# Kernel optimization log

Measured on AMD Instinct MI355X. Metric: run time of the kernel, lower is better.

The kernel has to match this reference:

```python
import jax, jax.numpy as jnp
import numpy as np

N_EMBD = 768
N_HEAD = 12
HEAD_SIZE = N_EMBD // N_HEAD
LN_EPS = 1e-5


def setup_inputs() -> dict:
    key = jax.random.key(0)
    ks = jax.random.split(key, 12)
    s = 0.02
    B, T, C = 8, 1024, N_EMBD
    return {
        "x":  jax.random.normal(ks[0], (B, T, C), dtype=jnp.float32),
        # per-head q/k/v projections packed as [C, H*hs] (concat of head outputs)
        "Wq": jax.random.normal(ks[1], (C, C), dtype=jnp.float32) * s,
        "Wk": jax.random.normal(ks[2], (C, C), dtype=jnp.float32) * s,
        "Wv": jax.random.normal(ks[3], (C, C), dtype=jnp.float32) * s,
        "Wo": jax.random.normal(ks[4], (C, C), dtype=jnp.float32) * s,
        "bo": jnp.zeros((C,), dtype=jnp.float32),
        "W1": jax.random.normal(ks[5], (C, 4 * C), dtype=jnp.float32) * s,
        "b1": jnp.zeros((4 * C,), dtype=jnp.float32),
        "W2": jax.random.normal(ks[6], (4 * C, C), dtype=jnp.float32) * s,
        "b2": jnp.zeros((C,), dtype=jnp.float32),
        "g1": jnp.ones((C,), dtype=jnp.float32),
        "be1": jnp.zeros((C,), dtype=jnp.float32),
        "g2": jnp.ones((C,), dtype=jnp.float32),
        "be2": jnp.zeros((C,), dtype=jnp.float32),
    }


def _layernorm(x, g, b):
    mu = jnp.mean(x, axis=-1, keepdims=True)
    var = jnp.mean(jnp.square(x - mu), axis=-1, keepdims=True)
    return (x - mu) * jax.lax.rsqrt(var + LN_EPS) * g + b


def _block(x, Wq, Wk, Wv, Wo, bo, W1, b1, W2, b2, g1, be1, g2, be2):
    B, T, C = x.shape
    H, hs = N_HEAD, HEAD_SIZE
    h = _layernorm(x, g1, be1)
    q = (h @ Wq).reshape(B, T, H, hs)
    k = (h @ Wk).reshape(B, T, H, hs)
    v = (h @ Wv).reshape(B, T, H, hs)
    # NOTE: original code scales by n_embd**-0.5 (C from x.shape), not head_size**-0.5
    scores = jnp.einsum("bthd,bshd->bhts", q, k) * (C ** -0.5)
    causal = jnp.tril(jnp.ones((T, T), dtype=bool))  # [T,T]
    scores = jnp.where(causal, scores, -jnp.inf)
    attn = jax.nn.softmax(scores, axis=-1)  # [B,H,T,T]
    o = jnp.einsum("bhts,bshd->bthd", attn, v).reshape(B, T, C)
    x = x + o @ Wo + bo
    h2 = _layernorm(x, g2, be2)
    ff = jax.nn.gelu(h2 @ W1 + b1, approximate=False) @ W2 + b2
    return x + ff


def reference(x, Wq, Wk, Wv, Wo, bo, W1, b1, W2, b2, g1, be1, g2, be2):
    return _block(x, Wq, Wk, Wv, Wo, bo, W1, b1, W2, b2, g1, be1, g2, be2)
```

## Files before the change

kernel.cpp:

```cpp
#include <hip/hip_runtime.h>
#include <math.h>
#include <stdint.h>

typedef unsigned short u16;
typedef unsigned int u32;
typedef __attribute__((ext_vector_type(8))) __bf16 bf16x8;
typedef __attribute__((ext_vector_type(4))) float f32x4;

#define AS1 __attribute__((address_space(1)))
#define AS3 __attribute__((address_space(3)))

__device__ __forceinline__ void stage16(const void* g, void* l) {
    __builtin_amdgcn_global_load_lds((const AS1 void*)(uintptr_t)g,
                                     (AS3 void*)(uintptr_t)l, 16, 0, 0);
}

__device__ __forceinline__ u16 f2bf(float f) {
    u32 u = __float_as_uint(f);
    u += 0x7fffu + ((u >> 16) & 1u);
    return (u16)(u >> 16);
}

__device__ __forceinline__ float bf2f(u16 v) {
    u32 u = ((u32)v) << 16;
    return __uint_as_float(u);
}

__global__ __launch_bounds__(256) void ln_kernel(const float* __restrict__ x,
                                                 const float* __restrict__ g,
                                                 const float* __restrict__ b,
                                                 u16* __restrict__ out) {
    __shared__ float s8[8];
    int row = blockIdx.x;
    int tid = threadIdx.x;
    const int w = tid >> 6;
    const float* xr = x + (size_t)row * 768;
    float x0 = xr[tid], x1 = xr[tid + 256], x2 = xr[tid + 512];

    float sum = x0 + x1 + x2;
#pragma unroll
    for (int off = 32; off; off >>= 1) sum += __shfl_xor(sum, off);
    if ((tid & 63) == 0) s8[w] = sum;
    __syncthreads();
    float mu = (s8[0] + s8[1] + s8[2] + s8[3]) * (1.0f / 768.0f);

    float d0 = x0 - mu, d1 = x1 - mu, d2 = x2 - mu;
    float sq = d0 * d0 + d1 * d1 + d2 * d2;
#pragma unroll
    for (int off = 32; off; off >>= 1) sq += __shfl_xor(sq, off);
    if ((tid & 63) == 0) s8[4 + w] = sq;
    __syncthreads();
    float var = (s8[4] + s8[5] + s8[6] + s8[7]) * (1.0f / 768.0f);
    float rs = rsqrtf(var + 1e-5f);

    u16* orow = out + (size_t)row * 768;
    orow[tid]       = f2bf(d0 * rs * g[tid]       + b[tid]);
    orow[tid + 256] = f2bf(d1 * rs * g[tid + 256] + b[tid + 256]);
    orow[tid + 512] = f2bf(d2 * rs * g[tid + 512] + b[tid + 512]);
}

__global__ __launch_bounds__(256) void transpose_bf16(const float* __restrict__ W,
                                                      u16* __restrict__ Wt,
                                                      int K, int N) {
    __shared__ float t[32][33];
    int tx = threadIdx.x, ty = threadIdx.y;
    int n0 = blockIdx.x * 32, k0 = blockIdx.y * 32;
#pragma unroll
    for (int j = 0; j < 32; j += 8)
        t[ty + j][tx] = W[(size_t)(k0 + ty + j) * N + n0 + tx];
    __syncthreads();
#pragma unroll
    for (int j = 0; j < 32; j += 8)
        Wt[(size_t)(n0 + ty + j) * K + k0 + tx] = f2bf(t[tx][ty + j]);
}

__global__ __launch_bounds__(256) void transpose4_768(const float* __restrict__ Wq,
                                                      const float* __restrict__ Wk,
                                                      const float* __restrict__ Wv,
                                                      const float* __restrict__ Wo,
                                                      u16* __restrict__ Wqkvt,
                                                      u16* __restrict__ Wot) {
    __shared__ float t[32][33];
    const int z = blockIdx.z;
    const float* W = (z == 0) ? Wq : (z == 1) ? Wk : (z == 2) ? Wv : Wo;
    u16* Wt = (z == 3) ? Wot : (Wqkvt + (size_t)z * 768 * 768);
    int tx = threadIdx.x, ty = threadIdx.y;
    int n0 = blockIdx.x * 32, k0 = blockIdx.y * 32;
#pragma unroll
    for (int j = 0; j < 32; j += 8)
        t[ty + j][tx] = W[(size_t)(k0 + ty + j) * 768 + n0 + tx];
    __syncthreads();
#pragma unroll
    for (int j = 0; j < 32; j += 8)
        Wt[(size_t)(n0 + ty + j) * 768 + k0 + tx] = f2bf(t[tx][ty + j]);
}

__global__ __launch_bounds__(256) void vt_kernel(const u16* __restrict__ qkv,
                                                 u16* __restrict__ Vt) {
    __shared__ u16 t[32][34];
    const int tx = threadIdx.x, ty = threadIdx.y;
    const int s0 = blockIdx.x * 32, d0 = blockIdx.y * 32, bh = blockIdx.z;
    const int b = bh / 12, h = bh % 12;
#pragma unroll
    for (int j = 0; j < 32; j += 8)
        t[ty + j][tx] = qkv[((size_t)(b * 1024) + s0 + ty + j) * 2304 + 1536 + h * 64 + d0 + tx];
    __syncthreads();
#pragma unroll
    for (int j = 0; j < 32; j += 8)
        Vt[((size_t)bh * 64 + d0 + ty + j) * 1024 + s0 + tx] = t[tx][ty + j];
}

__global__ __launch_bounds__(256, 3) void gemm_k32(
    const u16* __restrict__ A, const u16* __restrict__ Bt,
    const float* __restrict__ bias, const float* __restrict__ res,
    float* __restrict__ outF, u16* __restrict__ outB,
    int N, int K, int act) {
    __shared__ char lds[49152];
    const int tid = threadIdx.x, lane = tid & 63, wid = tid >> 6;
    const int l15 = lane & 15, lk = lane >> 4;
    const int wrow = (wid >> 1) * 64, wcol = (wid & 1) * 64;

    int wg = blockIdx.y * gridDim.x + blockIdx.x;
    const int nwg = gridDim.x * gridDim.y;
    wg = (wg & 7) * (nwg >> 3) + (wg >> 3);
    const int brow = (wg / gridDim.x) * 128;
    const int bcol = (wg % gridDim.x) * 128;

    const size_t K2 = (size_t)K * 2;
    const char* Abase = (const char*)A + (size_t)brow * K2;
    const char* Bbase = (const char*)Bt + (size_t)bcol * K2;

    int srow[2], scol[2];
#pragma unroll
    for (int j = 0; j < 2; ++j) {
        const int L = j * 4096 + tid * 16;
        srow[j] = L >> 6;
        scol[j] = (L & 63) ^ (((srow[j] >> 1) & 3) << 4);
    }

    const int nt = K >> 5;

    auto stage_tile = [&](int t, char* dst) {
#pragma unroll
        for (int j = 0; j < 2; ++j) {
            const size_t off = (size_t)srow[j] * K2 + (size_t)t * 64 + scol[j];
            stage16(Abase + off, dst + j * 4096 + tid * 16);
            stage16(Bbase + off, dst + 8192 + j * 4096 + tid * 16);
        }
    };

    f32x4 acc[4][4] = {};

    stage_tile(0, lds);
    stage_tile(1, lds + 16384);

    auto iter = [&](int t, char* buf, char* nxt) {
        if (t + 1 < nt) asm volatile("s_waitcnt vmcnt(4)\n\ts_barrier" ::: "memory");
        else            asm volatile("s_waitcnt vmcnt(0)\n\ts_barrier" ::: "memory");
        __builtin_amdgcn_sched_barrier(0);

        if (t + 2 < nt) stage_tile(t + 2, nxt);

        const char* As = buf;
        const char* Bs = buf + 8192;
        bf16x8 af[4], bfv[4];
#pragma unroll
        for (int m = 0; m < 4; ++m) {
            const int row = wrow + m * 16 + l15;
            af[m] = *(const bf16x8*)(As + row * 64 +
                                     ((lk * 16) ^ (((row >> 1) & 3) << 4)));
        }
#pragma unroll
        for (int n = 0; n < 4; ++n) {
            const int row = wcol + n * 16 + l15;
            bfv[n] = *(const bf16x8*)(Bs + row * 64 +
                                      ((lk * 16) ^ (((row >> 1) & 3) << 4)));
        }
        __builtin_amdgcn_s_setprio(1);
#pragma unroll
        for (int m = 0; m < 4; ++m)
#pragma unroll
            for (int n = 0; n < 4; ++n)
                acc[m][n] = __builtin_amdgcn_mfma_f32_16x16x32_bf16(af[m], bfv[n], acc[m][n], 0, 0, 0);
        __builtin_amdgcn_s_setprio(0);
    };

    for (int t = 0; t < nt; t += 3) {
        iter(t,     lds,         lds + 32768);
        iter(t + 1, lds + 16384, lds);
        iter(t + 2, lds + 32768, lds + 16384);
    }

#pragma unroll
    for (int m = 0; m < 4; ++m)
#pragma unroll
        for (int n = 0; n < 4; ++n)
#pragma unroll
            for (int r = 0; r < 4; ++r) {
                int row = brow + wrow + m * 16 + lk * 4 + r;
                int col = bcol + wcol + n * 16 + l15;
                float v = acc[m][n][r];
                if (bias) v += bias[col];
                if (act) v = 0.5f * v * (1.0f + erff(v * 0.70710678118654752f));
                if (res) v += res[(size_t)row * N + col];
                if (outB) outB[(size_t)row * N + col] = f2bf(v);
                else outF[(size_t)row * N + col] = v;
            }
}

__global__ __launch_bounds__(256, 3) void gemm_splitk(
    const u16* __restrict__ A, const u16* __restrict__ Bt,
    u16* __restrict__ p0, u16* __restrict__ p1, int N, int K) {
    __shared__ char lds[49152];
    const int tid = threadIdx.x, lane = tid & 63, wid = tid >> 6;
    const int l15 = lane & 15, lk = lane >> 4;
    const int wrow = (wid >> 1) * 64, wcol = (wid & 1) * 64;
    const int z = blockIdx.z;
    const int Kh = K >> 1;

    int wg = blockIdx.y * gridDim.x + blockIdx.x;
    const int nwg = gridDim.x * gridDim.y;
    wg = (wg & 7) * (nwg >> 3) + (wg >> 3);
    const int brow = (wg / gridDim.x) * 128;
    const int bcol = (wg % gridDim.x) * 128;

    const size_t K2 = (size_t)K * 2;
    const char* Abase = (const char*)A + (size_t)brow * K2 + (size_t)z * Kh * 2;
    const char* Bbase = (const char*)Bt + (size_t)bcol * K2 + (size_t)z * Kh * 2;

    int srow[2], scol[2];
#pragma unroll
    for (int j = 0; j < 2; ++j) {
        const int L = j * 4096 + tid * 16;
        srow[j] = L >> 6;
        scol[j] = (L & 63) ^ (((srow[j] >> 1) & 3) << 4);
    }

    const int nt = Kh >> 5;

    auto stage_tile = [&](int t, char* dst) {
#pragma unroll
        for (int j = 0; j < 2; ++j) {
            const size_t off = (size_t)srow[j] * K2 + (size_t)t * 64 + scol[j];
            stage16(Abase + off, dst + j * 4096 + tid * 16);
            stage16(Bbase + off, dst + 8192 + j * 4096 + tid * 16);
        }
    };

    f32x4 acc[4][4] = {};

    stage_tile(0, lds);
    stage_tile(1, lds + 16384);

    auto iter = [&](int t, char* buf, char* nxt) {
        if (t + 1 < nt) asm volatile("s_waitcnt vmcnt(4)\n\ts_barrier" ::: "memory");
        else            asm volatile("s_waitcnt vmcnt(0)\n\ts_barrier" ::: "memory");
        __builtin_amdgcn_sched_barrier(0);

        if (t + 2 < nt) stage_tile(t + 2, nxt);

        const char* As = buf;
        const char* Bs = buf + 8192;
        bf16x8 af[4], bfv[4];
#pragma unroll
        for (int m = 0; m < 4; ++m) {
            const int row = wrow + m * 16 + l15;
            af[m] = *(const bf16x8*)(As + row * 64 +
                                     ((lk * 16) ^ (((row >> 1) & 3) << 4)));
        }
#pragma unroll
        for (int n = 0; n < 4; ++n) {
            const int row = wcol + n * 16 + l15;
            bfv[n] = *(const bf16x8*)(Bs + row * 64 +
                                      ((lk * 16) ^ (((row >> 1) & 3) << 4)));
        }
        __builtin_amdgcn_s_setprio(1);
#pragma unroll
        for (int m = 0; m < 4; ++m)
#pragma unroll
            for (int n = 0; n < 4; ++n)
                acc[m][n] = __builtin_amdgcn_mfma_f32_16x16x32_bf16(af[m], bfv[n], acc[m][n], 0, 0, 0);
        __builtin_amdgcn_s_setprio(0);
    };

    for (int t = 0; t < nt; t += 3) {
        iter(t,     lds,         lds + 32768);
        iter(t + 1, lds + 16384, lds);
        iter(t + 2, lds + 32768, lds + 16384);
    }

    u16* outP = z ? p1 : p0;
#pragma unroll
    for (int m = 0; m < 4; ++m)
#pragma unroll
        for (int n = 0; n < 4; ++n)
#pragma unroll
            for (int r = 0; r < 4; ++r) {
                int row = brow + wrow + m * 16 + lk * 4 + r;
                int col = bcol + wcol + n * 16 + l15;
                outP[(size_t)row * N + col] = f2bf(acc[m][n][r]);
            }
}

__global__ __launch_bounds__(256) void ff2_reduce(const float* __restrict__ x2,
                                                  const float* __restrict__ b2,
                                                  const u16* __restrict__ p0,
                                                  const u16* __restrict__ p1,
                                                  float* __restrict__ out) {
    const size_t i = ((size_t)blockIdx.x * 256 + threadIdx.x) * 4;
    const float4 a = *(const float4*)(x2 + i);
    const int col = (int)(i % 768);
    const float4 bb = *(const float4*)(b2 + col);
    const ushort4 q0 = *(const ushort4*)(p0 + i);
    const ushort4 q1 = *(const ushort4*)(p1 + i);
    float4 o;
    o.x = a.x + bb.x + bf2f(q0.x) + bf2f(q1.x);
    o.y = a.y + bb.y + bf2f(q0.y) + bf2f(q1.y);
    o.z = a.z + bb.z + bf2f(q0.z) + bf2f(q1.z);
    o.w = a.w + bb.w + bf2f(q0.w) + bf2f(q1.w);
    *(float4*)(out + i) = o;
}

__global__ __launch_bounds__(256) void attn_mfma(const u16* __restrict__ qkv,
                                                 const u16* __restrict__ Vt,
                                                 u16* __restrict__ obf) {
    __shared__ char lds[40960];
    const int tid = threadIdx.x, lane = tid & 63, w = tid >> 6;
    const int g = lane >> 4, l15 = lane & 15;

    int wg = blockIdx.y * gridDim.x + blockIdx.x;
    const int nwg = gridDim.x * gridDim.y;
    wg = (wg & 7) * (nwg >> 3) + (wg >> 3);
    const int qb = 15 - (wg & 15);
    const int bh = wg >> 4;
    const int h = bh % 12, b = bh / 12;
    const int t0 = qb * 64;
    const float scale = 0.03608439182435161f;

    const size_t qrow = ((size_t)b * 1024 + t0 + 16 * w + l15) * 2304 + h * 64;
    const bf16x8 qf0 = *(const bf16x8*)(qkv + qrow + 8 * g);
    const bf16x8 qf1 = *(const bf16x8*)(qkv + qrow + 8 * g + 32);

    const int sub = ((lane & 7) * 16) ^ ((lane >> 3) << 4);
    const int r0 = 16 * w + (lane >> 3);
    const char* kSrc = (const char*)qkv + ((size_t)(b * 1024 + r0) * 2304 + 768 + h * 64) * 2 + sub;
    const char* vSrc = (const char*)Vt + ((size_t)(bh * 64 + r0) * 1024) * 2 + sub;
    const int dstOff = 2 * w * 1024 + lane * 16;

    stage16(kSrc,            lds + dstOff);
    stage16(kSrc + 8 * 4608, lds + dstOff + 1024);
    stage16(vSrc,            lds + 8192 + dstOff);
    stage16(vSrc + 8 * 2048, lds + 8192 + dstOff + 1024);
    kSrc += 64 * 4608; vSrc += 128;
    __syncthreads();

    const int swzA = (l15 & 7) << 4;
    float m_r[4] = {-1e30f, -1e30f, -1e30f, -1e30f};
    float l_r[4] = {0.f, 0.f, 0.f, 0.f};
    f32x4 oacc[4] = {};
    char* Pw = lds + 32768 + w * 2048;

    for (int c = 0; c <= qb; ++c) {
        if (c < qb) {
            char* dst = lds + ((c + 1) & 1) * 16384;
            stage16(kSrc,            dst + dstOff);
            stage16(kSrc + 8 * 4608, dst + dstOff + 1024);
            stage16(vSrc,            dst + 8192 + dstOff);
            stage16(vSrc + 8 * 2048, dst + 8192 + dstOff + 1024);
            kSrc += 64 * 4608; vSrc += 128;
            asm volatile("s_waitcnt vmcnt(4)\n\ts_barrier" ::: "memory");
        } else {
            asm volatile("s_waitcnt vmcnt(0)\n\ts_barrier" ::: "memory");
        }
        __builtin_amdgcn_sched_barrier(0);

        const char* bufK = lds + (c & 1) * 16384;
        const char* bufV = bufK + 8192;

        f32x4 sacc[4] = {};
#pragma unroll
        for (int st = 0; st < 4; ++st) {
            const char* krow = bufK + (l15 + 16 * st) * 128;
            const bf16x8 kf0 = *(const bf16x8*)(krow + ((16 * g) ^ swzA));
            const bf16x8 kf1 = *(const bf16x8*)(krow + ((16 * g + 64) ^ swzA));
            sacc[st] = __builtin_amdgcn_mfma_f32_16x16x32_bf16(qf0, kf0, sacc[st], 0, 0, 0);
            sacc[st] = __builtin_amdgcn_mfma_f32_16x16x32_bf16(qf1, kf1, sacc[st], 0, 0, 0);
        }

        const bool diag = (c == qb);
#pragma unroll
        for (int r = 0; r < 4; ++r) {
            float sv0 = sacc[0][r] * scale, sv1 = sacc[1][r] * scale;
            float sv2 = sacc[2][r] * scale, sv3 = sacc[3][r] * scale;
            if (diag) {
                const int trel = 16 * w + 4 * g + r;
                if (l15 +  0 > trel) sv0 = -1e30f;
                if (l15 + 16 > trel) sv1 = -1e30f;
                if (l15 + 32 > trel) sv2 = -1e30f;
                if (l15 + 48 > trel) sv3 = -1e30f;
            }
            float mx = fmaxf(fmaxf(sv0, sv1), fmaxf(sv2, sv3));
#pragma unroll
            for (int off = 1; off < 16; off <<= 1) mx = fmaxf(mx, __shfl_xor(mx, off));
            if (mx > m_r[r]) {
                const float corr = __expf(m_r[r] - mx);
                m_r[r] = mx;
                l_r[r] *= corr;
                oacc[0][r] *= corr; oacc[1][r] *= corr;
                oacc[2][r] *= corr; oacc[3][r] *= corr;
            }
            const float p0 = __expf(sv0 - m_r[r]), p1 = __expf(sv1 - m_r[r]);
            const float p2 = __expf(sv2 - m_r[r]), p3 = __expf(sv3 - m_r[r]);
            float ps = p0 + p1 + p2 + p3;
#pragma unroll
            for (int off = 1; off < 16; off <<= 1) ps += __shfl_xor(ps, off);
            l_r[r] += ps;
            const int q = 4 * g + r;
            char* pr = Pw + q * 128;
            const int sw = (q & 7) << 4;
            *(u16*)(pr + ((l15 * 2 +  0) ^ sw)) = f2bf(p0);
            *(u16*)(pr + ((l15 * 2 + 32) ^ sw)) = f2bf(p1);
            *(u16*)(pr + ((l15 * 2 + 64) ^ sw)) = f2bf(p2);
            *(u16*)(pr + ((l15 * 2 + 96) ^ sw)) = f2bf(p3);
        }

#pragma unroll
        for (int kc = 0; kc < 2; ++kc) {
            const bf16x8 pa = *(const bf16x8*)(Pw + l15 * 128 + ((16 * g + 64 * kc) ^ swzA));
#pragma unroll
            for (int dt = 0; dt < 4; ++dt) {
                const int d = l15 + 16 * dt;
                const bf16x8 vf = *(const bf16x8*)(bufV + d * 128 +
                                   ((16 * g + 64 * kc) ^ ((d & 7) << 4)));
                oacc[dt] = __builtin_amdgcn_mfma_f32_16x16x32_bf16(pa, vf, oacc[dt], 0, 0, 0);
            }
        }
        asm volatile("s_barrier" ::: "memory");
    }

    const size_t orow0 = ((size_t)b * 1024 + t0 + 16 * w) * 768 + h * 64;
#pragma unroll
    for (int r = 0; r < 4; ++r) {
        const float inv = 1.0f / l_r[r];
        const size_t orow = orow0 + (size_t)(4 * g + r) * 768;
#pragma unroll
        for (int dt = 0; dt < 4; ++dt)
            obf[orow + 16 * dt + l15] = f2bf(oacc[dt][r] * inv);
    }
}

extern "C" void kernel_launch(void* const* d_in, const int* in_sizes, int n_in,
                              void* d_out, int out_size, void* d_ws, size_t ws_size,
                              hipStream_t stream) {
    const float* x   = (const float*)d_in[0];
    const float* Wq  = (const float*)d_in[1];
    const float* Wk  = (const float*)d_in[2];
    const float* Wv  = (const float*)d_in[3];
    const float* Wo  = (const float*)d_in[4];
    const float* bo  = (const float*)d_in[5];
    const float* W1  = (const float*)d_in[6];
    const float* b1  = (const float*)d_in[7];
    const float* W2  = (const float*)d_in[8];
    const float* b2  = (const float*)d_in[9];
    const float* g1  = (const float*)d_in[10];
    const float* be1 = (const float*)d_in[11];
    const float* g2  = (const float*)d_in[12];
    const float* be2 = (const float*)d_in[13];
    float* out = (float*)d_out;

    char* ws = (char*)d_ws;
    u16* qkv_bf = (u16*)(ws);
    u16* ff1_bf = (u16*)(ws);
    float* x2   = (float*)(ws + 50331648);
    u16* h_bf   = (u16*)(ws + 75497472);
    u16* o_bf   = (u16*)(ws + 88080384);
    u16* p0_bf  = h_bf;
    u16* p1_bf  = o_bf;
    u16* Wqkvt  = (u16*)(ws + 100663296);
    u16* W1t    = (u16*)(ws + 104202240);
    u16* W2t    = (u16*)(ws + 108920832);
    u16* Wot    = (u16*)(ws + 113639424);
    u16* Vt     = (u16*)(ws + 114819072);

    dim3 tb(32, 8);
    transpose4_768<<<dim3(24, 24, 4), tb, 0, stream>>>(Wq, Wk, Wv, Wo, Wqkvt, Wot);
    transpose_bf16<<<dim3(96, 24), tb, 0, stream>>>(W1, W1t, 768, 3072);
    transpose_bf16<<<dim3(24, 96), tb, 0, stream>>>(W2, W2t, 3072, 768);

    ln_kernel<<<8192, 256, 0, stream>>>(x, g1, be1, h_bf);
    gemm_k32<<<dim3(18, 64), 256, 0, stream>>>(h_bf, Wqkvt, nullptr, nullptr, nullptr, qkv_bf, 2304, 768, 0);
    vt_kernel<<<dim3(32, 2, 96), tb, 0, stream>>>(qkv_bf, Vt);
    attn_mfma<<<dim3(16, 96), 256, 0, stream>>>(qkv_bf, Vt, o_bf);
    gemm_k32<<<dim3(6, 64), 256, 0, stream>>>(o_bf, Wot, bo, x, x2, nullptr, 768, 768, 0);
    ln_kernel<<<8192, 256, 0, stream>>>(x2, g2, be2, h_bf);
    gemm_k32<<<dim3(24, 64), 256, 0, stream>>>(h_bf, W1t, b1, nullptr, nullptr, ff1_bf, 3072, 768, 1);
    gemm_splitk<<<dim3(6, 64, 2), 256, 0, stream>>>(ff1_bf, W2t, p0_bf, p1_bf, 768, 3072);
    ff2_reduce<<<6144, 256, 0, stream>>>(x2, b2, p0_bf, p1_bf, out);
}
```

Baseline: 347.0 us.

## Pair causal query blocks per attention workgroup and widen FFN1 GEMM tile

The attention kernel now gives each workgroup two query blocks (p and 15-p) processed one after the other, so every workgroup does an equal amount of causal work and the grid is halved. A new gemm_x2 kernel computes a 128x256 output tile per workgroup for the W1 projection, reusing each A fragment across two B tiles and cutting the number of workgroups. The trade-offs are fewer workgroups with more serial work each, plus higher register pressure in gemm_x2 (two accumulator sets, launch bounds lowered to 2 waves per SIMD).

Result: faster. 330.3 us (-4.8%).

```diff
diff --git a/kernel.cpp b/kernel.cpp
--- a/kernel.cpp
+++ b/kernel.cpp
@@ -205,6 +205,117 @@
                 if (res) v += res[(size_t)row * N + col];
                 if (outB) outB[(size_t)row * N + col] = f2bf(v);
                 else outF[(size_t)row * N + col] = v;
+            }
+}
+
+__global__ __launch_bounds__(256, 2) void gemm_x2(
+    const u16* __restrict__ A, const u16* __restrict__ Bt,
+    const float* __restrict__ bias, u16* __restrict__ outB,
+    int N, int K, int act) {
+    __shared__ char lds[49152];
+    const int tid = threadIdx.x, lane = tid & 63, wid = tid >> 6;
+    const int l15 = lane & 15, lk = lane >> 4;
+    const int wrow = (wid >> 1) * 64, wcol = (wid & 1) * 64;
+
+    int wg = blockIdx.y * gridDim.x + blockIdx.x;
+    const int nwg = gridDim.x * gridDim.y;
+    wg = (wg & 7) * (nwg >> 3) + (wg >> 3);
+    const int brow = (wg / gridDim.x) * 128;
+    const int bcol = (wg % gridDim.x) * 256;
+
+    const size_t K2 = (size_t)K * 2;
+    const char* Abase  = (const char*)A + (size_t)brow * K2;
+    const char* B0base = (const char*)Bt + (size_t)bcol * K2;
+    const char* B1base = (const char*)Bt + (size_t)(bcol + 128) * K2;
+
+    int srow[2], scol[2];
+#pragma unroll
+    for (int j = 0; j < 2; ++j) {
+        const int L = j * 4096 + tid * 16;
+        srow[j] = L >> 6;
+        scol[j] = (L & 63) ^ (((srow[j] >> 1) & 3) << 4);
+    }
+
+    const int nt = K >> 5;
+
+    auto stage_tile = [&](int t, char* dst) {
+#pragma unroll
+        for (int j = 0; j < 2; ++j) {
+            const size_t off = (size_t)srow[j] * K2 + (size_t)t * 64 + scol[j];
+            stage16(Abase + off,  dst + j * 4096 + tid * 16);
+            stage16(B0base + off, dst + 8192 + j * 4096 + tid * 16);
+            stage16(B1base + off, dst + 16384 + j * 4096 + tid * 16);
+        }
+    };
+
+    f32x4 acc0[4][4] = {};
+    f32x4 acc1[4][4] = {};
+
+    stage_tile(0, lds);
+
+    for (int t = 0; t < nt; ++t) {
+        if (t + 1 < nt) {
+            stage_tile(t + 1, lds + ((t + 1) & 1) * 24576);
+            asm volatile("s_waitcnt vmcnt(6)\n\ts_barrier" ::: "memory");
+        } else {
+            asm volatile("s_waitcnt vmcnt(0)\n\ts_barrier" ::: "memory");
+        }
+        __builtin_amdgcn_sched_barrier(0);
+
+        const char* buf = lds + (t & 1) * 24576;
+        bf16x8 af[4], bfv[4];
+#pragma unroll
+        for (int m = 0; m < 4; ++m) {
+            const int row = wrow + m * 16 + l15;
+            af[m] = *(const bf16x8*)(buf + row * 64 +
+                                     ((lk * 16) ^ (((row >> 1) & 3) << 4)));
+        }
+#pragma unroll
+        for (int n = 0; n < 4; ++n) {
+            const int row = wcol + n * 16 + l15;
+            bfv[n] = *(const bf16x8*)(buf + 8192 + row * 64 +
+                                      ((lk * 16) ^ (((row >> 1) & 3) << 4)));
+        }
+        __builtin_amdgcn_s_setprio(1);
+#pragma unroll
+        for (int m = 0; m < 4; ++m)
+#pragma unroll
+            for (int n = 0; n < 4; ++n)
+                acc0[m][n] = __builtin_amdgcn_mfma_f32_16x16x32_bf16(af[m], bfv[n], acc0[m][n], 0, 0, 0);
+        __builtin_amdgcn_s_setprio(0);
+#pragma unroll
+        for (int n = 0; n < 4; ++n) {
+            const int row = wcol + n * 16 + l15;
+            bfv[n] = *(const bf16x8*)(buf + 16384 + row * 64 +
+                                      ((lk * 16) ^ (((row >> 1) & 3) << 4)));
+        }
+        __builtin_amdgcn_s_setprio(1);
+#pragma unroll
+        for (int m = 0; m < 4; ++m)
+#pragma unroll
+            for (int n = 0; n < 4; ++n)
+                acc1[m][n] = __builtin_amdgcn_mfma_f32_16x16x32_bf16(af[m], bfv[n], acc1[m][n], 0, 0, 0);
+        __builtin_amdgcn_s_setprio(0);
+        __builtin_amdgcn_s_barrier();
+    }
+
+#pragma unroll
+    for (int m = 0; m < 4; ++m)
+#pragma unroll
+        for (int n = 0; n < 4; ++n)
+#pragma unroll
+            for (int r = 0; r < 4; ++r) {
+                int row = brow + wrow + m * 16 + lk * 4 + r;
+                int col = bcol + wcol + n * 16 + l15;
+                float v0 = acc0[m][n][r];
+                float v1 = acc1[m][n][r];
+                if (bias) { v0 += bias[col]; v1 += bias[col + 128]; }
+                if (act) {
+                    v0 = 0.5f * v0 * (1.0f + erff(v0 * 0.70710678118654752f));
+                    v1 = 0.5f * v1 * (1.0f + erff(v1 * 0.70710678118654752f));
+                }
+                outB[(size_t)row * N + col]       = f2bf(v0);
+                outB[(size_t)row * N + col + 128] = f2bf(v1);
             }
 }
 
@@ -331,121 +442,127 @@
     int wg = blockIdx.y * gridDim.x + blockIdx.x;
     const int nwg = gridDim.x * gridDim.y;
     wg = (wg & 7) * (nwg >> 3) + (wg >> 3);
-    const int qb = 15 - (wg & 15);
-    const int bh = wg >> 4;
+    const int p = wg / 96;
+    const int bh = wg % 96;
     const int h = bh % 12, b = bh / 12;
-    const int t0 = qb * 64;
     const float scale = 0.03608439182435161f;
-
-    const size_t qrow = ((size_t)b * 1024 + t0 + 16 * w + l15) * 2304 + h * 64;
-    const bf16x8 qf0 = *(const bf16x8*)(qkv + qrow + 8 * g);
-    const bf16x8 qf1 = *(const bf16x8*)(qkv + qrow + 8 * g + 32);
 
     const int sub = ((lane & 7) * 16) ^ ((lane >> 3) << 4);
     const int r0 = 16 * w + (lane >> 3);
-    const char* kSrc = (const char*)qkv + ((size_t)(b * 1024 + r0) * 2304 + 768 + h * 64) * 2 + sub;
-    const char* vSrc = (const char*)Vt + ((size_t)(bh * 64 + r0) * 1024) * 2 + sub;
     const int dstOff = 2 * w * 1024 + lane * 16;
-
-    stage16(kSrc,            lds + dstOff);
-    stage16(kSrc + 8 * 4608, lds + dstOff + 1024);
-    stage16(vSrc,            lds + 8192 + dstOff);
-    stage16(vSrc + 8 * 2048, lds + 8192 + dstOff + 1024);
-    kSrc += 64 * 4608; vSrc += 128;
-    __syncthreads();
-
     const int swzA = (l15 & 7) << 4;
-    float m_r[4] = {-1e30f, -1e30f, -1e30f, -1e30f};
-    float l_r[4] = {0.f, 0.f, 0.f, 0.f};
-    f32x4 oacc[4] = {};
     char* Pw = lds + 32768 + w * 2048;
 
-    for (int c = 0; c <= qb; ++c) {
-        if (c < qb) {
-            char* dst = lds + ((c + 1) & 1) * 16384;
-            stage16(kSrc,            dst + dstOff);
-            stage16(kSrc + 8 * 4608, dst + dstOff + 1024);
-            stage16(vSrc,            dst + 8192 + dstOff);
-            stage16(vSrc + 8 * 2048, dst + 8192 + dstOff + 1024);
-            kSrc += 64 * 4608; vSrc += 128;
-            asm volatile("s_waitcnt vmcnt(4)\n\ts_barrier" ::: "memory");
-        } else {
-            asm volatile("s_waitcnt vmcnt(0)\n\ts_barrier" ::: "memory");
-        }
-        __builtin_amdgcn_sched_barrier(0);
-
-        const char* bufK = lds + (c & 1) * 16384;
-        const char* bufV = bufK + 8192;
-
-        f32x4 sacc[4] = {};
-#pragma unroll
-        for (int st = 0; st < 4; ++st) {
-            const char* krow = bufK + (l15 + 16 * st) * 128;
-            const bf16x8 kf0 = *(const bf16x8*)(krow + ((16 * g) ^ swzA));
-            const bf16x8 kf1 = *(const bf16x8*)(krow + ((16 * g + 64) ^ swzA));
-            sacc[st] = __builtin_amdgcn_mfma_f32_16x16x32_bf16(qf0, kf0, sacc[st], 0, 0, 0);
-            sacc[st] = __builtin_amdgcn_mfma_f32_16x16x32_bf16(qf1, kf1, sacc[st], 0, 0, 0);
-        }
-
-        const bool diag = (c == qb);
+#pragma unroll 1
+    for (int half = 0; half < 2; ++half) {
+        const int qb = half ? p : (15 - p);
+        const int t0 = qb * 64;
+
+        const size_t qrow = ((size_t)b * 1024 + t0 + 16 * w + l15) * 2304 + h * 64;
+        const bf16x8 qf0 = *(const bf16x8*)(qkv + qrow + 8 * g);
+        const bf16x8 qf1 = *(const bf16x8*)(qkv + qrow + 8 * g + 32);
+
+        const char* kSrc = (const char*)qkv + ((size_t)(b * 1024 + r0) * 2304 + 768 + h * 64) * 2 + sub;
+        const char* vSrc = (const char*)Vt + ((size_t)(bh * 64 + r0) * 1024) * 2 + sub;
+
+        stage16(kSrc,            lds + dstOff);
+        stage16(kSrc + 8 * 4608, lds + dstOff + 1024);
+        stage16(vSrc,            lds + 8192 + dstOff);
+        stage16(vSrc + 8 * 2048, lds + 8192 + dstOff + 1024);
+        kSrc += 64 * 4608; vSrc += 128;
+        __syncthreads();
+
+        float m_r[4] = {-1e30f, -1e30f, -1e30f, -1e30f};
+        float l_r[4] = {0.f, 0.f, 0.f, 0.f};
+        f32x4 oacc[4] = {};
+
+        for (int c = 0; c <= qb; ++c) {
+            if (c < qb) {
+                char* dst = lds + ((c + 1) & 1) * 16384;
+                stage16(kSrc,            dst + dstOff);
+                stage16(kSrc + 8 * 4608, dst + dstOff + 1024);
+                stage16(vSrc,            dst + 8192 + dstOff);
+                stage16(vSrc + 8 * 2048, dst + 8192 + dstOff + 1024);
+                kSrc += 64 * 4608; vSrc += 128;
+                asm volatile("s_waitcnt vmcnt(4)\n\ts_barrier" ::: "memory");
+            } else {
+                asm volatile("s_waitcnt vmcnt(0)\n\ts_barrier" ::: "memory");
+            }
+            __builtin_amdgcn_sched_barrier(0);
+
+            const char* bufK = lds + (c & 1) * 16384;
+            const char* bufV = bufK + 8192;
+
+            f32x4 sacc[4] = {};
+#pragma unroll
+            for (int st = 0; st < 4; ++st) {
+                const char* krow = bufK + (l15 + 16 * st) * 128;
+                const bf16x8 kf0 = *(const bf16x8*)(krow + ((16 * g) ^ swzA));
+                const bf16x8 kf1 = *(const bf16x8*)(krow + ((16 * g + 64) ^ swzA));
+                sacc[st] = __builtin_amdgcn_mfma_f32_16x16x32_bf16(qf0, kf0, sacc[st], 0, 0, 0);
+                sacc[st] = __builtin_amdgcn_mfma_f32_16x16x32_bf16(qf1, kf1, sacc[st], 0, 0, 0);
+            }
+
+            const bool diag = (c == qb);
+#pragma unroll
+            for (int r = 0; r < 4; ++r) {
+                float sv0 = sacc[0][r] * scale, sv1 = sacc[1][r] * scale;
+                float sv2 = sacc[2][r] * scale, sv3 = sacc[3][r] * scale;
+                if (diag) {
+                    const int trel = 16 * w + 4 * g + r;
+                    if (l15 +  0 > trel) sv0 = -1e30f;
+                    if (l15 + 16 > trel) sv1 = -1e30f;
+                    if (l15 + 32 > trel) sv2 = -1e30f;
+                    if (l15 + 48 > trel) sv3 = -1e30f;
+                }
+                float mx = fmaxf(fmaxf(sv0, sv1), fmaxf(sv2, sv3));
+#pragma unroll
+                for (int off = 1; off < 16; off <<= 1) mx = fmaxf(mx, __shfl_xor(mx, off));
+                if (mx > m_r[r]) {
+                    const float corr = __expf(m_r[r] - mx);
+                    m_r[r] = mx;
+                    l_r[r] *= corr;
+                    oacc[0][r] *= corr; oacc[1][r] *= corr;
+                    oacc[2][r] *= corr; oacc[3][r] *= corr;
+                }
+                const float p0 = __expf(sv0 - m_r[r]), p1 = __expf(sv1 - m_r[r]);
+                const float p2 = __expf(sv2 - m_r[r]), p3 = __expf(sv3 - m_r[r]);
+                float ps = p0 + p1 + p2 + p3;
+#pragma unroll
+                for (int off = 1; off < 16; off <<= 1) ps += __shfl_xor(ps, off);
+                l_r[r] += ps;
+                const int q = 4 * g + r;
+                char* pr = Pw + q * 128;
+                const int sw = (q & 7) << 4;
+                *(u16*)(pr + ((l15 * 2 +  0) ^ sw)) = f2bf(p0);
+                *(u16*)(pr + ((l15 * 2 + 32) ^ sw)) = f2bf(p1);
+                *(u16*)(pr + ((l15 * 2 + 64) ^ sw)) = f2bf(p2);
+                *(u16*)(pr + ((l15 * 2 + 96) ^ sw)) = f2bf(p3);
+            }
+
+#pragma unroll
+            for (int kc = 0; kc < 2; ++kc) {
+                const bf16x8 pa = *(const bf16x8*)(Pw + l15 * 128 + ((16 * g + 64 * kc) ^ swzA));
+#pragma unroll
+                for (int dt = 0; dt < 4; ++dt) {
+                    const int d = l15 + 16 * dt;
+                    const bf16x8 vf = *(const bf16x8*)(bufV + d * 128 +
+                                       ((16 * g + 64 * kc) ^ ((d & 7) << 4)));
+                    oacc[dt] = __builtin_amdgcn_mfma_f32_16x16x32_bf16(pa, vf, oacc[dt], 0, 0, 0);
+                }
+            }
+            asm volatile("s_barrier" ::: "memory");
+        }
+
+        const size_t orow0 = ((size_t)b * 1024 + t0 + 16 * w) * 768 + h * 64;
 #pragma unroll
         for (int r = 0; r < 4; ++r) {
-            float sv0 = sacc[0][r] * scale, sv1 = sacc[1][r] * scale;
-            float sv2 = sacc[2][r] * scale, sv3 = sacc[3][r] * scale;
-            if (diag) {
-                const int trel = 16 * w + 4 * g + r;
-                if (l15 +  0 > trel) sv0 = -1e30f;
-                if (l15 + 16 > trel) sv1 = -1e30f;
-                if (l15 + 32 > trel) sv2 = -1e30f;
-                if (l15 + 48 > trel) sv3 = -1e30f;
-            }
-            float mx = fmaxf(fmaxf(sv0, sv1), fmaxf(sv2, sv3));
-#pragma unroll
-            for (int off = 1; off < 16; off <<= 1) mx = fmaxf(mx, __shfl_xor(mx, off));
-            if (mx > m_r[r]) {
-                const float corr = __expf(m_r[r] - mx);
-                m_r[r] = mx;
-                l_r[r] *= corr;
-                oacc[0][r] *= corr; oacc[1][r] *= corr;
-                oacc[2][r] *= corr; oacc[3][r] *= corr;
-            }
-            const float p0 = __expf(sv0 - m_r[r]), p1 = __expf(sv1 - m_r[r]);
-            const float p2 = __expf(sv2 - m_r[r]), p3 = __expf(sv3 - m_r[r]);
-            float ps = p0 + p1 + p2 + p3;
-#pragma unroll
-            for (int off = 1; off < 16; off <<= 1) ps += __shfl_xor(ps, off);
-            l_r[r] += ps;
-            const int q = 4 * g + r;
-            char* pr = Pw + q * 128;
-            const int sw = (q & 7) << 4;
-            *(u16*)(pr + ((l15 * 2 +  0) ^ sw)) = f2bf(p0);
-            *(u16*)(pr + ((l15 * 2 + 32) ^ sw)) = f2bf(p1);
-            *(u16*)(pr + ((l15 * 2 + 64) ^ sw)) = f2bf(p2);
-            *(u16*)(pr + ((l15 * 2 + 96) ^ sw)) = f2bf(p3);
-        }
-
-#pragma unroll
-        for (int kc = 0; kc < 2; ++kc) {
-            const bf16x8 pa = *(const bf16x8*)(Pw + l15 * 128 + ((16 * g + 64 * kc) ^ swzA));
-#pragma unroll
-            for (int dt = 0; dt < 4; ++dt) {
-                const int d = l15 + 16 * dt;
-                const bf16x8 vf = *(const bf16x8*)(bufV + d * 128 +
-                                   ((16 * g + 64 * kc) ^ ((d & 7) << 4)));
-                oacc[dt] = __builtin_amdgcn_mfma_f32_16x16x32_bf16(pa, vf, oacc[dt], 0, 0, 0);
-            }
-        }
-        asm volatile("s_barrier" ::: "memory");
-    }
-
-    const size_t orow0 = ((size_t)b * 1024 + t0 + 16 * w) * 768 + h * 64;
-#pragma unroll
-    for (int r = 0; r < 4; ++r) {
-        const float inv = 1.0f / l_r[r];
-        const size_t orow = orow0 + (size_t)(4 * g + r) * 768;
-#pragma unroll
-        for (int dt = 0; dt < 4; ++dt)
-            obf[orow + 16 * dt + l15] = f2bf(oacc[dt][r] * inv);
+            const float inv = 1.0f / l_r[r];
+            const size_t orow = orow0 + (size_t)(4 * g + r) * 768;
+#pragma unroll
+            for (int dt = 0; dt < 4; ++dt)
+                obf[orow + 16 * dt + l15] = f2bf(oacc[dt][r] * inv);
+        }
     }
 }
 
@@ -490,10 +607,10 @@
     ln_kernel<<<8192, 256, 0, stream>>>(x, g1, be1, h_bf);
     gemm_k32<<<dim3(18, 64), 256, 0, stream>>>(h_bf, Wqkvt, nullptr, nullptr, nullptr, qkv_bf, 2304, 768, 0);
     vt_kernel<<<dim3(32, 2, 96), tb, 0, stream>>>(qkv_bf, Vt);
-    attn_mfma<<<dim3(16, 96), 256, 0, stream>>>(qkv_bf, Vt, o_bf);
+    attn_mfma<<<dim3(8, 96), 256, 0, stream>>>(qkv_bf, Vt, o_bf);
     gemm_k32<<<dim3(6, 64), 256, 0, stream>>>(o_bf, Wot, bo, x, x2, nullptr, 768, 768, 0);
     ln_kernel<<<8192, 256, 0, stream>>>(x2, g2, be2, h_bf);
-    gemm_k32<<<dim3(24, 64), 256, 0, stream>>>(h_bf, W1t, b1, nullptr, nullptr, ff1_bf, 3072, 768, 1);
+    gemm_x2<<<dim3(12, 64), 256, 0, stream>>>(h_bf, W1t, b1, ff1_bf, 3072, 768, 1);
     gemm_splitk<<<dim3(6, 64, 2), 256, 0, stream>>>(ff1_bf, W2t, p0_bf, p1_bf, 768, 3072);
     ff2_reduce<<<6144, 256, 0, stream>>>(x2, b2, p0_bf, p1_bf, out);
 }
```

## Pair causal query blocks per workgroup and stage GEMM bf16 epilogues through LDS

Applied to the files above, without the earlier changes.

The attention kernel now gives each workgroup two query blocks, p and 15-p, processed one after the other. This balances the causal triangle's work across workgroups and halves the grid. The bf16-output GEMM epilogues (gemm_k32 with outB, and split-K) now write the tile into LDS first, then store it to global memory as coalesced 16-byte rows instead of scattered 2-byte stores. The cost is an extra LDS round trip and a barrier, a longer serial loop per attention workgroup, and fewer attention workgroups to fill the GPU.

New measurement: 308.2 us. -11.2%, faster.

```diff
diff --git a/kernel.cpp b/kernel.cpp
--- a/kernel.cpp
+++ b/kernel.cpp
@@ -191,21 +191,45 @@
         iter(t + 2, lds + 32768, lds + 16384);
     }
 
-#pragma unroll
-    for (int m = 0; m < 4; ++m)
-#pragma unroll
-        for (int n = 0; n < 4; ++n)
-#pragma unroll
-            for (int r = 0; r < 4; ++r) {
-                int row = brow + wrow + m * 16 + lk * 4 + r;
-                int col = bcol + wcol + n * 16 + l15;
-                float v = acc[m][n][r];
-                if (bias) v += bias[col];
-                if (act) v = 0.5f * v * (1.0f + erff(v * 0.70710678118654752f));
-                if (res) v += res[(size_t)row * N + col];
-                if (outB) outB[(size_t)row * N + col] = f2bf(v);
-                else outF[(size_t)row * N + col] = v;
-            }
+    if (outB) {
+        u16* ctile = (u16*)lds;
+#pragma unroll
+        for (int m = 0; m < 4; ++m)
+#pragma unroll
+            for (int n = 0; n < 4; ++n)
+#pragma unroll
+                for (int r = 0; r < 4; ++r) {
+                    float v = acc[m][n][r];
+                    int col = wcol + n * 16 + l15;
+                    if (bias) v += bias[bcol + col];
+                    if (act) v = 0.5f * v * (1.0f + erff(v * 0.70710678118654752f));
+                    ctile[(wrow + m * 16 + lk * 4 + r) * 128 + col] = f2bf(v);
+                }
+        __syncthreads();
+#pragma unroll
+        for (int pass = 0; pass < 8; ++pass) {
+            const int idx = pass * 256 + tid;
+            const int row = idx >> 4;
+            const int seg = idx & 15;
+            *(bf16x8*)(outB + (size_t)(brow + row) * N + bcol + seg * 8) =
+                *(const bf16x8*)(ctile + row * 128 + seg * 8);
+        }
+    } else {
+#pragma unroll
+        for (int m = 0; m < 4; ++m)
+#pragma unroll
+            for (int n = 0; n < 4; ++n)
+#pragma unroll
+                for (int r = 0; r < 4; ++r) {
+                    int row = brow + wrow + m * 16 + lk * 4 + r;
+                    int col = bcol + wcol + n * 16 + l15;
+                    float v = acc[m][n][r];
+                    if (bias) v += bias[col];
+                    if (act) v = 0.5f * v * (1.0f + erff(v * 0.70710678118654752f));
+                    if (res) v += res[(size_t)row * N + col];
+                    outF[(size_t)row * N + col] = v;
+                }
+    }
 }
 
 __global__ __launch_bounds__(256, 3) void gemm_splitk(
@@ -290,16 +314,24 @@
     }
 
     u16* outP = z ? p1 : p0;
+    u16* ctile = (u16*)lds;
 #pragma unroll
     for (int m = 0; m < 4; ++m)
 #pragma unroll
         for (int n = 0; n < 4; ++n)
 #pragma unroll
-            for (int r = 0; r < 4; ++r) {
-                int row = brow + wrow + m * 16 + lk * 4 + r;
-                int col = bcol + wcol + n * 16 + l15;
-                outP[(size_t)row * N + col] = f2bf(acc[m][n][r]);
-            }
+            for (int r = 0; r < 4; ++r)
+                ctile[(wrow + m * 16 + lk * 4 + r) * 128 + wcol + n * 16 + l15] =
+                    f2bf(acc[m][n][r]);
+    __syncthreads();
+#pragma unroll
+    for (int pass = 0; pass < 8; ++pass) {
+        const int idx = pass * 256 + tid;
+        const int row = idx >> 4;
+        const int seg = idx & 15;
+        *(bf16x8*)(outP + (size_t)(brow + row) * N + bcol + seg * 8) =
+            *(const bf16x8*)(ctile + row * 128 + seg * 8);
+    }
 }
 
 __global__ __launch_bounds__(256) void ff2_reduce(const float* __restrict__ x2,
@@ -331,121 +363,127 @@
     int wg = blockIdx.y * gridDim.x + blockIdx.x;
     const int nwg = gridDim.x * gridDim.y;
     wg = (wg & 7) * (nwg >> 3) + (wg >> 3);
-    const int qb = 15 - (wg & 15);
-    const int bh = wg >> 4;
+    const int p = wg / 96;
+    const int bh = wg % 96;
     const int h = bh % 12, b = bh / 12;
-    const int t0 = qb * 64;
     const float scale = 0.03608439182435161f;
-
-    const size_t qrow = ((size_t)b * 1024 + t0 + 16 * w + l15) * 2304 + h * 64;
-    const bf16x8 qf0 = *(const bf16x8*)(qkv + qrow + 8 * g);
-    const bf16x8 qf1 = *(const bf16x8*)(qkv + qrow + 8 * g + 32);
 
     const int sub = ((lane & 7) * 16) ^ ((lane >> 3) << 4);
     const int r0 = 16 * w + (lane >> 3);
-    const char* kSrc = (const char*)qkv + ((size_t)(b * 1024 + r0) * 2304 + 768 + h * 64) * 2 + sub;
-    const char* vSrc = (const char*)Vt + ((size_t)(bh * 64 + r0) * 1024) * 2 + sub;
     const int dstOff = 2 * w * 1024 + lane * 16;
-
-    stage16(kSrc,            lds + dstOff);
-    stage16(kSrc + 8 * 4608, lds + dstOff + 1024);
-    stage16(vSrc,            lds + 8192 + dstOff);
-    stage16(vSrc + 8 * 2048, lds + 8192 + dstOff + 1024);
-    kSrc += 64 * 4608; vSrc += 128;
-    __syncthreads();
-
     const int swzA = (l15 & 7) << 4;
-    float m_r[4] = {-1e30f, -1e30f, -1e30f, -1e30f};
-    float l_r[4] = {0.f, 0.f, 0.f, 0.f};
-    f32x4 oacc[4] = {};
     char* Pw = lds + 32768 + w * 2048;
 
-    for (int c = 0; c <= qb; ++c) {
-        if (c < qb) {
-            char* dst = lds + ((c + 1) & 1) * 16384;
-            stage16(kSrc,            dst + dstOff);
-            stage16(kSrc + 8 * 4608, dst + dstOff + 1024);
-            stage16(vSrc,            dst + 8192 + dstOff);
-            stage16(vSrc + 8 * 2048, dst + 8192 + dstOff + 1024);
-            kSrc += 64 * 4608; vSrc += 128;
-            asm volatile("s_waitcnt vmcnt(4)\n\ts_barrier" ::: "memory");
-        } else {
-            asm volatile("s_waitcnt vmcnt(0)\n\ts_barrier" ::: "memory");
-        }
-        __builtin_amdgcn_sched_barrier(0);
-
-        const char* bufK = lds + (c & 1) * 16384;
-        const char* bufV = bufK + 8192;
-
-        f32x4 sacc[4] = {};
-#pragma unroll
-        for (int st = 0; st < 4; ++st) {
-            const char* krow = bufK + (l15 + 16 * st) * 128;
-            const bf16x8 kf0 = *(const bf16x8*)(krow + ((16 * g) ^ swzA));
-            const bf16x8 kf1 = *(const bf16x8*)(krow + ((16 * g + 64) ^ swzA));
-            sacc[st] = __builtin_amdgcn_mfma_f32_16x16x32_bf16(qf0, kf0, sacc[st], 0, 0, 0);
-            sacc[st] = __builtin_amdgcn_mfma_f32_16x16x32_bf16(qf1, kf1, sacc[st], 0, 0, 0);
-        }
-
-        const bool diag = (c == qb);
+#pragma unroll 1
+    for (int half = 0; half < 2; ++half) {
+        const int qb = half ? p : (15 - p);
+        const int t0 = qb * 64;
+
+        const size_t qrow = ((size_t)b * 1024 + t0 + 16 * w + l15) * 2304 + h * 64;
+        const bf16x8 qf0 = *(const bf16x8*)(qkv + qrow + 8 * g);
+        const bf16x8 qf1 = *(const bf16x8*)(qkv + qrow + 8 * g + 32);
+
+        const char* kSrc = (const char*)qkv + ((size_t)(b * 1024 + r0) * 2304 + 768 + h * 64) * 2 + sub;
+        const char* vSrc = (const char*)Vt + ((size_t)(bh * 64 + r0) * 1024) * 2 + sub;
+
+        stage16(kSrc,            lds + dstOff);
+        stage16(kSrc + 8 * 4608, lds + dstOff + 1024);
+        stage16(vSrc,            lds + 8192 + dstOff);
+        stage16(vSrc + 8 * 2048, lds + 8192 + dstOff + 1024);
+        kSrc += 64 * 4608; vSrc += 128;
+        __syncthreads();
+
+        float m_r[4] = {-1e30f, -1e30f, -1e30f, -1e30f};
+        float l_r[4] = {0.f, 0.f, 0.f, 0.f};
+        f32x4 oacc[4] = {};
+
+        for (int c = 0; c <= qb; ++c) {
+            if (c < qb) {
+                char* dst = lds + ((c + 1) & 1) * 16384;
+                stage16(kSrc,            dst + dstOff);
+                stage16(kSrc + 8 * 4608, dst + dstOff + 1024);
+                stage16(vSrc,            dst + 8192 + dstOff);
+                stage16(vSrc + 8 * 2048, dst + 8192 + dstOff + 1024);
+                kSrc += 64 * 4608; vSrc += 128;
+                asm volatile("s_waitcnt vmcnt(4)\n\ts_barrier" ::: "memory");
+            } else {
+                asm volatile("s_waitcnt vmcnt(0)\n\ts_barrier" ::: "memory");
+            }
+            __builtin_amdgcn_sched_barrier(0);
+
+            const char* bufK = lds + (c & 1) * 16384;
+            const char* bufV = bufK + 8192;
+
+            f32x4 sacc[4] = {};
+#pragma unroll
+            for (int st = 0; st < 4; ++st) {
+                const char* krow = bufK + (l15 + 16 * st) * 128;
+                const bf16x8 kf0 = *(const bf16x8*)(krow + ((16 * g) ^ swzA));
+                const bf16x8 kf1 = *(const bf16x8*)(krow + ((16 * g + 64) ^ swzA));
+                sacc[st] = __builtin_amdgcn_mfma_f32_16x16x32_bf16(qf0, kf0, sacc[st], 0, 0, 0);
+                sacc[st] = __builtin_amdgcn_mfma_f32_16x16x32_bf16(qf1, kf1, sacc[st], 0, 0, 0);
+            }
+
+            const bool diag = (c == qb);
+#pragma unroll
+            for (int r = 0; r < 4; ++r) {
+                float sv0 = sacc[0][r] * scale, sv1 = sacc[1][r] * scale;
+                float sv2 = sacc[2][r] * scale, sv3 = sacc[3][r] * scale;
+                if (diag) {
+                    const int trel = 16 * w + 4 * g + r;
+                    if (l15 +  0 > trel) sv0 = -1e30f;
+                    if (l15 + 16 > trel) sv1 = -1e30f;
+                    if (l15 + 32 > trel) sv2 = -1e30f;
+                    if (l15 + 48 > trel) sv3 = -1e30f;
+                }
+                float mx = fmaxf(fmaxf(sv0, sv1), fmaxf(sv2, sv3));
+#pragma unroll
+                for (int off = 1; off < 16; off <<= 1) mx = fmaxf(mx, __shfl_xor(mx, off));
+                if (mx > m_r[r]) {
+                    const float corr = __expf(m_r[r] - mx);
+                    m_r[r] = mx;
+                    l_r[r] *= corr;
+                    oacc[0][r] *= corr; oacc[1][r] *= corr;
+                    oacc[2][r] *= corr; oacc[3][r] *= corr;
+                }
+                const float p0 = __expf(sv0 - m_r[r]), p1 = __expf(sv1 - m_r[r]);
+                const float p2 = __expf(sv2 - m_r[r]), p3 = __expf(sv3 - m_r[r]);
+                float ps = p0 + p1 + p2 + p3;
+#pragma unroll
+                for (int off = 1; off < 16; off <<= 1) ps += __shfl_xor(ps, off);
+                l_r[r] += ps;
+                const int q = 4 * g + r;
+                char* pr = Pw + q * 128;
+                const int sw = (q & 7) << 4;
+                *(u16*)(pr + ((l15 * 2 +  0) ^ sw)) = f2bf(p0);
+                *(u16*)(pr + ((l15 * 2 + 32) ^ sw)) = f2bf(p1);
+                *(u16*)(pr + ((l15 * 2 + 64) ^ sw)) = f2bf(p2);
+                *(u16*)(pr + ((l15 * 2 + 96) ^ sw)) = f2bf(p3);
+            }
+
+#pragma unroll
+            for (int kc = 0; kc < 2; ++kc) {
+                const bf16x8 pa = *(const bf16x8*)(Pw + l15 * 128 + ((16 * g + 64 * kc) ^ swzA));
+#pragma unroll
+                for (int dt = 0; dt < 4; ++dt) {
+                    const int d = l15 + 16 * dt;
+                    const bf16x8 vf = *(const bf16x8*)(bufV + d * 128 +
+                                       ((16 * g + 64 * kc) ^ ((d & 7) << 4)));
+                    oacc[dt] = __builtin_amdgcn_mfma_f32_16x16x32_bf16(pa, vf, oacc[dt], 0, 0, 0);
+                }
+            }
+            asm volatile("s_barrier" ::: "memory");
+        }
+
+        const size_t orow0 = ((size_t)b * 1024 + t0 + 16 * w) * 768 + h * 64;
 #pragma unroll
         for (int r = 0; r < 4; ++r) {
-            float sv0 = sacc[0][r] * scale, sv1 = sacc[1][r] * scale;
-            float sv2 = sacc[2][r] * scale, sv3 = sacc[3][r] * scale;
-            if (diag) {
-                const int trel = 16 * w + 4 * g + r;
-                if (l15 +  0 > trel) sv0 = -1e30f;
-                if (l15 + 16 > trel) sv1 = -1e30f;
-                if (l15 + 32 > trel) sv2 = -1e30f;
-                if (l15 + 48 > trel) sv3 = -1e30f;
-            }
-            float mx = fmaxf(fmaxf(sv0, sv1), fmaxf(sv2, sv3));
-#pragma unroll
-            for (int off = 1; off < 16; off <<= 1) mx = fmaxf(mx, __shfl_xor(mx, off));
-            if (mx > m_r[r]) {
-                const float corr = __expf(m_r[r] - mx);
-                m_r[r] = mx;
-                l_r[r] *= corr;
-                oacc[0][r] *= corr; oacc[1][r] *= corr;
-                oacc[2][r] *= corr; oacc[3][r] *= corr;
-            }
-            const float p0 = __expf(sv0 - m_r[r]), p1 = __expf(sv1 - m_r[r]);
-            const float p2 = __expf(sv2 - m_r[r]), p3 = __expf(sv3 - m_r[r]);
-            float ps = p0 + p1 + p2 + p3;
-#pragma unroll
-            for (int off = 1; off < 16; off <<= 1) ps += __shfl_xor(ps, off);
-            l_r[r] += ps;
-            const int q = 4 * g + r;
-            char* pr = Pw + q * 128;
-            const int sw = (q & 7) << 4;
-            *(u16*)(pr + ((l15 * 2 +  0) ^ sw)) = f2bf(p0);
-            *(u16*)(pr + ((l15 * 2 + 32) ^ sw)) = f2bf(p1);
-            *(u16*)(pr + ((l15 * 2 + 64) ^ sw)) = f2bf(p2);
-            *(u16*)(pr + ((l15 * 2 + 96) ^ sw)) = f2bf(p3);
-        }
-
-#pragma unroll
-        for (int kc = 0; kc < 2; ++kc) {
-            const bf16x8 pa = *(const bf16x8*)(Pw + l15 * 128 + ((16 * g + 64 * kc) ^ swzA));
-#pragma unroll
-            for (int dt = 0; dt < 4; ++dt) {
-                const int d = l15 + 16 * dt;
-                const bf16x8 vf = *(const bf16x8*)(bufV + d * 128 +
-                                   ((16 * g + 64 * kc) ^ ((d & 7) << 4)));
-                oacc[dt] = __builtin_amdgcn_mfma_f32_16x16x32_bf16(pa, vf, oacc[dt], 0, 0, 0);
-            }
-        }
-        asm volatile("s_barrier" ::: "memory");
-    }
-
-    const size_t orow0 = ((size_t)b * 1024 + t0 + 16 * w) * 768 + h * 64;
-#pragma unroll
-    for (int r = 0; r < 4; ++r) {
-        const float inv = 1.0f / l_r[r];
-        const size_t orow = orow0 + (size_t)(4 * g + r) * 768;
-#pragma unroll
-        for (int dt = 0; dt < 4; ++dt)
-            obf[orow + 16 * dt + l15] = f2bf(oacc[dt][r] * inv);
+            const float inv = 1.0f / l_r[r];
+            const size_t orow = orow0 + (size_t)(4 * g + r) * 768;
+#pragma unroll
+            for (int dt = 0; dt < 4; ++dt)
+                obf[orow + 16 * dt + l15] = f2bf(oacc[dt][r] * inv);
+        }
     }
 }
 
@@ -490,7 +528,7 @@
     ln_kernel<<<8192, 256, 0, stream>>>(x, g1, be1, h_bf);
     gemm_k32<<<dim3(18, 64), 256, 0, stream>>>(h_bf, Wqkvt, nullptr, nullptr, nullptr, qkv_bf, 2304, 768, 0);
     vt_kernel<<<dim3(32, 2, 96), tb, 0, stream>>>(qkv_bf, Vt);
-    attn_mfma<<<dim3(16, 96), 256, 0, stream>>>(qkv_bf, Vt, o_bf);
+    attn_mfma<<<dim3(8, 96), 256, 0, stream>>>(qkv_bf, Vt, o_bf);
     gemm_k32<<<dim3(6, 64), 256, 0, stream>>>(o_bf, Wot, bo, x, x2, nullptr, 768, 768, 0);
     ln_kernel<<<8192, 256, 0, stream>>>(x2, g2, be2, h_bf);
     gemm_k32<<<dim3(24, 64), 256, 0, stream>>>(h_bf, W1t, b1, nullptr, nullptr, ff1_bf, 3072, 768, 1);
```
